# Kernel tuning notes

Hardware: AMD Instinct MI355X
Metric: run time of the kernel (lower is better)

The kernel has to match this reference:

```python
import jax, jax.numpy as jnp
import numpy as np

B, CIN, H, W = 4, 128, 160, 160
K = 100          # num instances
CH = 8           # mask head channels
OUT = 8          # mask branch out channels
STRIDE = 4
EPS = 1e-5


def conv3x3(x, w):
    # x: [B,C,H,W], w: [O,C,3,3] -> [B,O,H,W], stride 1, pad 1
    return jax.lax.conv_general_dilated(x, w, (1, 1), 'SAME',
                                        dimension_numbers=('NCHW', 'OIHW', 'NCHW'))


def setup_inputs() -> dict:
    key = jax.random.key(0)
    ks = jax.random.split(key, 6)
    cnn_feature = jax.random.normal(ks[0], (B, CIN, H, W), jnp.float32)
    tower_w = jax.random.normal(ks[1], (4, 128, 128, 3, 3), jnp.float32) * 0.03
    bn_gamma = jnp.ones((4, 128), jnp.float32)
    bn_beta = jnp.zeros((4, 128), jnp.float32)
    bn_mean = jnp.zeros((4, 128), jnp.float32)
    bn_var = jnp.ones((4, 128), jnp.float32)
    proj_w = jax.random.normal(ks[2], (OUT, 128), jnp.float32) * 0.05
    proj_b = jnp.zeros((OUT,), jnp.float32)
    ctrl_w = jax.random.normal(ks[3], (169, CIN, 3, 3), jnp.float32) * 0.01
    ctrl_b = jnp.zeros((169,), jnp.float32)
    detection = jax.random.randint(ks[4], (K, 2), 0, min(H, W), dtype=jnp.int32)
    return dict(cnn_feature=cnn_feature, tower_w=tower_w, bn_gamma=bn_gamma,
                bn_beta=bn_beta, bn_mean=bn_mean, bn_var=bn_var,
                proj_w=proj_w, proj_b=proj_b, ctrl_w=ctrl_w, ctrl_b=ctrl_b,
                detection=detection)


def reference(cnn_feature, tower_w, bn_gamma, bn_beta, bn_mean, bn_var,
              proj_w, proj_b, ctrl_w, ctrl_b, detection):
    x = cnn_feature
    for i in range(4):
        x = conv3x3(x, tower_w[i])
        inv = bn_gamma[i] / jnp.sqrt(bn_var[i] + EPS)            # [128]
        shift = bn_beta[i] - bn_mean[i] * inv
        x = jax.nn.relu(x * inv[None, :, None, None] + shift[None, :, None, None])
    mask_feats = jnp.einsum('bchw,oc->bohw', x, proj_w) + proj_b[None, :, None, None]

    # ----- controller: 3x3 conv producing 169 dynamic params per pixel -----
    ctrl = conv3x3(cnn_feature, ctrl_w) + ctrl_b[None, :, None, None]  # [B,169,H,W]

    # ----- gather per-instance params at detection centers (im_inds all 0) -----
    xs = detection[:, 0]
    ys = detection[:, 1]
    params = ctrl[0][:, ys, xs].T  # [K,169]

    # ----- relative coordinates -----
    sx = jnp.arange(W, dtype=jnp.float32) * STRIDE + STRIDE // 2
    sy = jnp.arange(H, dtype=jnp.float32) * STRIDE + STRIDE // 2
    gy, gx = jnp.meshgrid(sy, sx, indexing='ij')
    locations = jnp.stack([gx.reshape(-1), gy.reshape(-1)], axis=1)   # [HW,2]
    ct = detection.astype(jnp.float32) * STRIDE                        # [K,2]
    rel = (ct[:, None, :] - locations[None, :, :]).transpose(0, 2, 1)  # [K,2,HW]

    feats = jnp.broadcast_to(mask_feats[0].reshape(1, OUT, H * W), (K, OUT, H * W))
    h = jnp.concatenate([rel, feats], axis=1)  # [K,10,HW]

    # ----- parse dynamic params: weights first, then biases -----
    w0 = params[:, 0:80].reshape(K, CH, OUT + 2)     # (8+2)*8
    w1 = params[:, 80:144].reshape(K, CH, CH)        # 8*8
    w2 = params[:, 144:152].reshape(K, 1, CH)        # 8*1
    b0 = params[:, 152:160]
    b1 = params[:, 160:168]
    b2 = params[:, 168:169]

    # ----- dynamic grouped 1x1 convs == per-instance matmuls -----
    h = jax.nn.relu(jnp.einsum('koc,kcp->kop', w0, h) + b0[:, :, None])
    h = jax.nn.relu(jnp.einsum('koc,kcp->kop', w1, h) + b1[:, :, None])
    h = jnp.einsum('koc,kcp->kop', w2, h) + b2[:, :, None]  # [K,1,HW]
    return h.reshape(K, H, W)
```

## Files before the change

kernel.cpp:

```cpp
#include <hip/hip_runtime.h>
#include <hip/hip_bf16.h>

#define H 160
#define W 160
#define HW 25600
#define ROWB 40960

typedef __attribute__((ext_vector_type(8))) short bf16x8;
typedef __attribute__((ext_vector_type(4))) float f32x4;
typedef __attribute__((ext_vector_type(8))) unsigned short ushort8v;
typedef __attribute__((ext_vector_type(4))) unsigned short ushort4v;

typedef __attribute__((address_space(1))) const unsigned int gu32;
typedef __attribute__((address_space(3))) unsigned int lu32;

__device__ __forceinline__ void gload16(const void* g, void* l) {
    __builtin_amdgcn_global_load_lds((gu32*)g, (lu32*)l, 16, 0, 0);
}

__device__ __forceinline__ unsigned short f2b(float f) {
    unsigned int u = __float_as_uint(f);
    unsigned int r = (u + 0x7fffu + ((u >> 16) & 1u)) >> 16;
    return (unsigned short)r;
}
__device__ __forceinline__ float b2f(unsigned short b) {
    return __uint_as_float(((unsigned int)b) << 16);
}

#define LGKM0() asm volatile("s_waitcnt lgkmcnt(0)" ::: "memory")
#define BARRIER() asm volatile("s_barrier" ::: "memory")


__global__ __launch_bounds__(256) void fused_prep(
    const float* __restrict__ cnn,
    const float* __restrict__ tw,
    const float* __restrict__ gamma, const float* __restrict__ beta,
    const float* __restrict__ mean,  const float* __restrict__ var,
    const float* __restrict__ cw,
    char* __restrict__ actX, char* __restrict__ wbf,
    float* __restrict__ invshift, float* __restrict__ cwT)
{
    const int tid = threadIdx.x;
    const int b = blockIdx.x;

    if (b < 200) {
        int blk = b;
        int p0  = blk * 128 + (tid & 31) * 4;
        int cbh = tid >> 5;
#pragma unroll
        for (int pass = 0; pass < 2; ++pass) {
            int cb2 = pass * 8 + cbh;
            int ci0 = cb2 * 8;
            ushort8v o0, o1, o2, o3;
#pragma unroll
            for (int jj = 0; jj < 8; ++jj) {
                float4 v = *(const float4*)&cnn[(ci0 + jj) * HW + p0];
                o0[jj] = f2b(v.x);
                o1[jj] = f2b(v.y);
                o2[jj] = f2b(v.z);
                o3[jj] = f2b(v.w);
            }
            *(ushort8v*)(actX + (p0 + 0) * 256 + ((cb2 ^ ((p0 + 0) & 15)) * 16)) = o0;
            *(ushort8v*)(actX + (p0 + 1) * 256 + ((cb2 ^ ((p0 + 1) & 15)) * 16)) = o1;
            *(ushort8v*)(actX + (p0 + 2) * 256 + ((cb2 ^ ((p0 + 2) & 15)) * 16)) = o2;
            *(ushort8v*)(actX + (p0 + 3) * 256 + ((cb2 ^ ((p0 + 3) & 15)) * 16)) = o3;
        }
    } else if (b < 456) {
        int idx = (b - 200) * 256 + tid;
        int ci = idx & 127;
        int co = (idx >> 7) & 127;
        int l  = idx >> 14;
        int kk = ci >> 5;
        int cw2 = ci & 31;
        const float* src = tw + ((l * 128 + co) * 128 + ci) * 9;
        char* dst = wbf + l * 294912 + kk * 8192 + co * 64 + cw2 * 2;
#pragma unroll
        for (int t = 0; t < 9; ++t)
            *(unsigned short*)(dst + t * 32768) = f2b(src[t]);

        if (b == 200) {
            for (int c = tid; c < 512; c += 256) {
                int ll = c >> 7, ch = c & 127;
                float inv = gamma[ll * 128 + ch] * rsqrtf(var[ll * 128 + ch] + 1e-5f);
                float sh  = beta[ll * 128 + ch] - mean[ll * 128 + ch] * inv;
                invshift[ll * 256 + ch] = inv;
                invshift[ll * 256 + 128 + ch] = sh;
            }
        }
    } else {
        int idx = (b - 456) * 256 + tid;
        if (idx < 194688) {
            int j = idx / 169;
            int o = idx - j * 169;
            cwT[idx] = cw[o * 1152 + j];
        }
    }
}

template <int PROJ, int CTRL>
__global__ __launch_bounds__(512, 1) void conv_mfma(
    const char* __restrict__ actin,
    const char* __restrict__ wpl,
    const float* __restrict__ invshift_l,
    char* __restrict__ actout,
    const float* __restrict__ pw,
    const float* __restrict__ pb,
    float* __restrict__ mf,
    const float* __restrict__ cnn,
    const float* __restrict__ cwT,
    const float* __restrict__ cbp,
    const int*   __restrict__ det,
    float* __restrict__ params)
{
    __shared__ __align__(16) char smem[78848];

    const int tid  = threadIdx.x;

    if (CTRL && blockIdx.x >= 200) {
        float* patch = (float*)smem;
        float* sred  = (float*)(smem + 4608);
        const int k = blockIdx.x - 200;
        const int xk = det[2 * k];
        const int yk = det[2 * k + 1];
        for (int i = tid; i < 1152; i += 512) {
            int ci = i / 9;
            int rem = i - ci * 9;
            int r = rem / 3, s = rem - r * 3;
            int gy = yk + r - 1, gx = xk + s - 1;
            float v = 0.f;
            if ((unsigned)gy < (unsigned)H && (unsigned)gx < (unsigned)W)
                v = cnn[ci * HW + gy * W + gx];
            patch[i] = v;
        }
        __syncthreads();

        float acc = 0.f;
        if (tid < 507) {
            const int chunk = tid / 169;
            const int o = tid - chunk * 169;
            const int j0 = chunk * 384;
            const float* cp = cwT + o;
#pragma unroll 8
            for (int j = j0; j < j0 + 384; ++j)
                acc += cp[j * 169] * patch[j];
        }
        if (tid >= 169 && tid < 507) sred[tid - 169] = acc;
        __syncthreads();
        if (tid < 169)
            params[k * 169 + tid] = acc + sred[tid] + sred[169 + tid] + cbp[tid];
        return;
    }

    char* IT = smem;
    char* WQ = smem + 46080;

    const int lane = tid & 63;
    const int w    = tid >> 6;
    const int wp   = w >> 1;
    const int wc   = w & 1;
    const int g    = lane >> 4;
    const int i15  = lane & 15;

    const int bb = blockIdx.x;
    const int bx = bb % 10;
    const int by = bb / 10;
    const int tx0 = bx * 16 - 1;
    const int ty0 = by * 8 - 1;

    for (int it = 0; it < 6; ++it) {
        int c = it * 512 + tid;
        if (c < 2880) {
            int row  = c / 288;
            int rem  = c - row * 288;
            int px_i = rem >> 4;
            int bo   = (rem & 15) * 16;
            int cy = min(max(ty0 + row, 0), H - 1);
            int cx = min(max(tx0 + px_i, 0), W - 1);
            char* ldsb = IT + (it * 512 + (tid & ~63)) * 16;
            gload16(actin + cy * ROWB + cx * 256 + bo, ldsb);
        }
    }
#pragma unroll
    for (int pl = 0; pl < 3; ++pl)
        gload16(wpl + pl * 8192 + tid * 16,
                WQ + pl * 8192 + (tid & ~63) * 16);
    asm volatile("s_waitcnt vmcnt(2)" ::: "memory");
    for (int c = tid; c < 2880; c += 512) {
        int row  = c / 288;
        int rem  = c - row * 288;
        int px_i = rem >> 4;
        int gy = ty0 + row, gx = tx0 + px_i;
        if ((unsigned)gy >= (unsigned)H || (unsigned)gx >= (unsigned)W) {
            f32x4 z = {0.f, 0.f, 0.f, 0.f};
            *(f32x4*)(IT + c * 16) = z;
        }
    }
    LGKM0();
    BARRIER();

    f32x4 acc[4][2];
#pragma unroll
    for (int cf = 0; cf < 4; ++cf)
#pragma unroll
        for (int pf = 0; pf < 2; ++pf)
            acc[cf][pf] = (f32x4){0.f, 0.f, 0.f, 0.f};

#define CSTAGE(J, WN) {                                                        \
    if ((J) <= 32)                                                             \
        gload16(wpl + ((J) + 3) * 8192 + tid * 16,                             \
                WQ + (((J) + 3) & 3) * 8192 + (tid & ~63) * 16);               \
    asm volatile("s_waitcnt vmcnt(" #WN ")" ::: "memory");                     \
    {                                                                          \
        const int tap = (J) >> 2, kk = (J) & 3;                                \
        const int r = tap / 3, s = tap - r * 3;                                \
        const char* wbse = WQ + ((J) & 3) * 8192 + (wc * 64 + i15) * 64 + g * 16; \
        bf16x8 a0 = *(const bf16x8*)(wbse + 0 * 1024);                         \
        bf16x8 a1 = *(const bf16x8*)(wbse + 1 * 1024);                         \
        bf16x8 a2 = *(const bf16x8*)(wbse + 2 * 1024);                         \
        bf16x8 a3 = *(const bf16x8*)(wbse + 3 * 1024);                         \
        const int slotb = ((kk * 4 + g) ^ ((i15 + s + 15) & 15)) * 16;         \
        const char* ib = IT + (i15 + s) * 256 + slotb;                         \
        bf16x8 b0 = *(const bf16x8*)(ib + (wp * 2 + 0 + r) * 4608);            \
        bf16x8 b1 = *(const bf16x8*)(ib + (wp * 2 + 1 + r) * 4608);            \
        acc[0][0] = __builtin_amdgcn_mfma_f32_16x16x32_bf16(a0, b0, acc[0][0], 0, 0, 0); \
        acc[0][1] = __builtin_amdgcn_mfma_f32_16x16x32_bf16(a0, b1, acc[0][1], 0, 0, 0); \
        acc[1][0] = __builtin_amdgcn_mfma_f32_16x16x32_bf16(a1, b0, acc[1][0], 0, 0, 0); \
        acc[1][1] = __builtin_amdgcn_mfma_f32_16x16x32_bf16(a1, b1, acc[1][1], 0, 0, 0); \
        acc[2][0] = __builtin_amdgcn_mfma_f32_16x16x32_bf16(a2, b0, acc[2][0], 0, 0, 0); \
        acc[2][1] = __builtin_amdgcn_mfma_f32_16x16x32_bf16(a2, b1, acc[2][1], 0, 0, 0); \
        acc[3][0] = __builtin_amdgcn_mfma_f32_16x16x32_bf16(a3, b0, acc[3][0], 0, 0, 0); \
        acc[3][1] = __builtin_amdgcn_mfma_f32_16x16x32_bf16(a3, b1, acc[3][1], 0, 0, 0); \
    }                                                                          \
    BARRIER();                                                                 \
}

    CSTAGE(0,2)  CSTAGE(1,2)  CSTAGE(2,2)  CSTAGE(3,2)  CSTAGE(4,2)  CSTAGE(5,2)
    CSTAGE(6,2)  CSTAGE(7,2)  CSTAGE(8,2)  CSTAGE(9,2)  CSTAGE(10,2) CSTAGE(11,2)
    CSTAGE(12,2) CSTAGE(13,2) CSTAGE(14,2) CSTAGE(15,2) CSTAGE(16,2) CSTAGE(17,2)
    CSTAGE(18,2) CSTAGE(19,2) CSTAGE(20,2) CSTAGE(21,2) CSTAGE(22,2) CSTAGE(23,2)
    CSTAGE(24,2) CSTAGE(25,2) CSTAGE(26,2) CSTAGE(27,2) CSTAGE(28,2) CSTAGE(29,2)
    CSTAGE(30,2) CSTAGE(31,2) CSTAGE(32,2) CSTAGE(33,1) CSTAGE(34,0) CSTAGE(35,0)
#undef CSTAGE

    if (PROJ == 0) {
        const int gx = bx * 16 + i15;
#pragma unroll
        for (int cf = 0; cf < 4; ++cf) {
            int co0 = wc * 64 + cf * 16 + g * 4;
            int cbx = wc * 8 + cf * 2 + (g >> 1);
            int sbyte = ((cbx ^ i15) * 16) + (g & 1) * 8;
            f32x4 inv4 = *(const f32x4*)&invshift_l[co0];
            f32x4 sh4  = *(const f32x4*)&invshift_l[128 + co0];
#pragma unroll
            for (int pf = 0; pf < 2; ++pf) {
                int gy = by * 8 + wp * 2 + pf;
                f32x4 v = acc[cf][pf];
                ushort4v o;
                o.x = f2b(fmaxf(v.x * inv4.x + sh4.x, 0.f));
                o.y = f2b(fmaxf(v.y * inv4.y + sh4.y, 0.f));
                o.z = f2b(fmaxf(v.z * inv4.z + sh4.z, 0.f));
                o.w = f2b(fmaxf(v.w * inv4.w + sh4.w, 0.f));
                *(ushort4v*)(actout + gy * ROWB + gx * 256 + sbyte) = o;
            }
        }
    } else {
        char* actF = smem;
        float* spw = (float*)(smem + 32768);
        __syncthreads();
#pragma unroll
        for (int cf = 0; cf < 4; ++cf) {
            int co0 = wc * 64 + cf * 16 + g * 4;
            int cbx = wc * 8 + cf * 2 + (g >> 1);
            int sbyte = ((cbx ^ i15) * 16) + (g & 1) * 8;
            f32x4 inv4 = *(const f32x4*)&invshift_l[co0];
            f32x4 sh4  = *(const f32x4*)&invshift_l[128 + co0];
#pragma unroll
            for (int pf = 0; pf < 2; ++pf) {
                int px = (wp * 2 + pf) * 16 + i15;
                f32x4 v = acc[cf][pf];
                ushort4v o;
                o.x = f2b(fmaxf(v.x * inv4.x + sh4.x, 0.f));
                o.y = f2b(fmaxf(v.y * inv4.y + sh4.y, 0.f));
                o.z = f2b(fmaxf(v.z * inv4.z + sh4.z, 0.f));
                o.w = f2b(fmaxf(v.w * inv4.w + sh4.w, 0.f));
                *(ushort4v*)(actF + px * 256 + sbyte) = o;
            }
        }
        for (int i = tid; i < 1024; i += 512) spw[i] = pw[i];
        __syncthreads();
        int pxt = tid >> 2;
        int o0  = (tid & 3) * 2;
        float s0 = 0.f, s1 = 0.f;
#pragma unroll
        for (int cb2 = 0; cb2 < 16; ++cb2) {
            ushort8v vv = *(const ushort8v*)(actF + pxt * 256 + ((cb2 ^ (pxt & 15)) * 16));
#pragma unroll
            for (int j = 0; j < 8; ++j) {
                float f = b2f(vv[j]);
                int ci = cb2 * 8 + j;
                s0 += f * spw[o0 * 128 + ci];
                s1 += f * spw[(o0 + 1) * 128 + ci];
            }
        }
        int p = (by * 8 + (pxt >> 4)) * W + bx * 16 + (pxt & 15);
        mf[o0 * HW + p]       = s0 + pb[o0];
        mf[(o0 + 1) * HW + p] = s1 + pb[o0 + 1];
    }
}

__global__ __launch_bounds__(256) void head_kernel(
    const float* __restrict__ mf, const float* __restrict__ params,
    const int* __restrict__ det, float* __restrict__ out)
{
    __shared__ float sp[1690];
    __shared__ int sdet[20];
    const int tid = threadIdx.x;
    const int kg = blockIdx.y;
    for (int i = tid; i < 1690; i += 256) sp[i] = params[kg * 1690 + i];
    if (tid < 20) sdet[tid] = det[kg * 20 + tid];
    __syncthreads();

    const int p = blockIdx.x * 256 + tid;
    const int x = p % W;
    const int y = p / W;
    const float fx = (float)(x * 4 + 2);
    const float fy = (float)(y * 4 + 2);

    float f[8];
#pragma unroll
    for (int o = 0; o < 8; ++o) f[o] = mf[o * HW + p];

#pragma unroll 2
    for (int j = 0; j < 10; ++j) {
        const float* spj = &sp[j * 169];
        const float rel0 = (float)(sdet[2 * j] * 4) - fx;
        const float rel1 = (float)(sdet[2 * j + 1] * 4) - fy;
        float h0[8];
#pragma unroll
        for (int o = 0; o < 8; ++o) {
            float a = spj[152 + o] + spj[o * 10] * rel0 + spj[o * 10 + 1] * rel1;
#pragma unroll
            for (int c = 0; c < 8; ++c) a += spj[o * 10 + 2 + c] * f[c];
            h0[o] = fmaxf(a, 0.f);
        }
        float h1[8];
#pragma unroll
        for (int o = 0; o < 8; ++o) {
            float a = spj[160 + o];
#pragma unroll
            for (int c = 0; c < 8; ++c) a += spj[80 + o * 8 + c] * h0[c];
            h1[o] = fmaxf(a, 0.f);
        }
        float r = spj[168];
#pragma unroll
        for (int c = 0; c < 8; ++c) r += spj[144 + c] * h1[c];
        out[(kg * 10 + j) * HW + p] = r;
    }
}

extern "C" void kernel_launch(void* const* d_in, const int* in_sizes, int n_in,
                              void* d_out, int out_size, void* d_ws, size_t ws_size,
                              hipStream_t stream)
{
    const float* cnn    = (const float*)d_in[0];
    const float* towerw = (const float*)d_in[1];
    const float* gamma  = (const float*)d_in[2];
    const float* beta   = (const float*)d_in[3];
    const float* meanp  = (const float*)d_in[4];
    const float* varp   = (const float*)d_in[5];
    const float* projw  = (const float*)d_in[6];
    const float* projb  = (const float*)d_in[7];
    const float* ctrlw  = (const float*)d_in[8];
    const float* ctrlb  = (const float*)d_in[9];
    const int*   det    = (const int*)d_in[10];
    float* out = (float*)d_out;

    char*  outb     = (char*)d_out;
    char*  X        = outb;
    char*  wbf      = outb + 6553600;
    float* invshift = (float*)(outb + 7733248);
    float* cwT      = (float*)(outb + 7737344);

    char*  Y      = (char*)d_ws;
    float* mf     = (float*)((char*)d_ws + 6553600);
    float* params = (float*)((char*)d_ws + 7372800);

    fused_prep<<<dim3(1217), dim3(256), 0, stream>>>(
        cnn, towerw, gamma, beta, meanp, varp, ctrlw,
        X, wbf, invshift, cwT);

    conv_mfma<0, 1><<<dim3(300), dim3(512), 0, stream>>>(
        X, wbf + 0 * 294912, invshift + 0 * 256, Y,
        nullptr, nullptr, nullptr,
        cnn, cwT, ctrlb, det, params);
    conv_mfma<0, 0><<<dim3(200), dim3(512), 0, stream>>>(
        Y, wbf + 1 * 294912, invshift + 1 * 256, X,
        nullptr, nullptr, nullptr,
        nullptr, nullptr, nullptr, nullptr, nullptr);
    conv_mfma<0, 0><<<dim3(200), dim3(512), 0, stream>>>(
        X, wbf + 2 * 294912, invshift + 2 * 256, Y,
        nullptr, nullptr, nullptr,
        nullptr, nullptr, nullptr, nullptr, nullptr);
    conv_mfma<1, 0><<<dim3(200), dim3(512), 0, stream>>>(
        Y, wbf + 3 * 294912, invshift + 3 * 256, nullptr,
        projw, projb, mf,
        nullptr, nullptr, nullptr, nullptr, nullptr);

    head_kernel<<<dim3(100, 10), dim3(256), 0, stream>>>(mf, params, det, out);
}
```

Before: 103.9 us.

## Fuse dynamic mask head into last tower conv epilogue, drop head kernel

Folds the per-instance dynamic head computation into the epilogue of the final tower conv kernel. Mask features now stay in shared memory instead of round-tripping through global memory, and one kernel launch is removed. Because the output buffer is now written during that kernel, the layer-4 weights and BN params are moved into workspace so they are not overwritten. The trade-off is that the 200 conv blocks must each stream all 100 instance parameter sets, in five chunks separated by barriers, which serializes the head work onto fewer blocks.

```diff
diff --git a/kernel.cpp b/kernel.cpp
--- a/kernel.cpp
+++ b/kernel.cpp
@@ -38,7 +38,8 @@
     const float* __restrict__ mean,  const float* __restrict__ var,
     const float* __restrict__ cw,
     char* __restrict__ actX, char* __restrict__ wbf,
-    float* __restrict__ invshift, float* __restrict__ cwT)
+    float* __restrict__ invshift, float* __restrict__ cwT,
+    char* __restrict__ wbf4, float* __restrict__ invshift4)
 {
     const int tid = threadIdx.x;
     const int b = blockIdx.x;
@@ -73,7 +74,8 @@
         int kk = ci >> 5;
         int cw2 = ci & 31;
         const float* src = tw + ((l * 128 + co) * 128 + ci) * 9;
-        char* dst = wbf + l * 294912 + kk * 8192 + co * 64 + cw2 * 2;
+        char* base = (l < 3) ? (wbf + l * 294912) : wbf4;
+        char* dst = base + kk * 8192 + co * 64 + cw2 * 2;
 #pragma unroll
         for (int t = 0; t < 9; ++t)
             *(unsigned short*)(dst + t * 32768) = f2b(src[t]);
@@ -85,6 +87,10 @@
                 float sh  = beta[ll * 128 + ch] - mean[ll * 128 + ch] * inv;
                 invshift[ll * 256 + ch] = inv;
                 invshift[ll * 256 + 128 + ch] = sh;
+                if (ll == 3) {
+                    invshift4[ch] = inv;
+                    invshift4[128 + ch] = sh;
+                }
             }
         }
     } else {
@@ -105,12 +111,12 @@
     char* __restrict__ actout,
     const float* __restrict__ pw,
     const float* __restrict__ pb,
-    float* __restrict__ mf,
     const float* __restrict__ cnn,
     const float* __restrict__ cwT,
     const float* __restrict__ cbp,
     const int*   __restrict__ det,
-    float* __restrict__ params)
+    float* __restrict__ params,
+    float* __restrict__ outp)
 {
     __shared__ __align__(16) char smem[78848];
 
@@ -264,8 +270,11 @@
             }
         }
     } else {
-        char* actF = smem;
-        float* spw = (float*)(smem + 32768);
+        char* actF  = smem;
+        float* spw  = (float*)(smem + 32768);
+        float* pmf  = (float*)(smem + 36864);
+        float* spar = (float*)(smem + 40960);
+        int*   sdet = (int*)(smem + 54480);
         __syncthreads();
 #pragma unroll
         for (int cf = 0; cf < 4; ++cf) {
@@ -287,74 +296,71 @@
             }
         }
         for (int i = tid; i < 1024; i += 512) spw[i] = pw[i];
+        for (int i = tid; i < 200; i += 512) sdet[i] = det[i];
         __syncthreads();
-        int pxt = tid >> 2;
-        int o0  = (tid & 3) * 2;
-        float s0 = 0.f, s1 = 0.f;
-#pragma unroll
-        for (int cb2 = 0; cb2 < 16; ++cb2) {
-            ushort8v vv = *(const ushort8v*)(actF + pxt * 256 + ((cb2 ^ (pxt & 15)) * 16));
-#pragma unroll
-            for (int j = 0; j < 8; ++j) {
-                float f = b2f(vv[j]);
-                int ci = cb2 * 8 + j;
-                s0 += f * spw[o0 * 128 + ci];
-                s1 += f * spw[(o0 + 1) * 128 + ci];
-            }
-        }
-        int p = (by * 8 + (pxt >> 4)) * W + bx * 16 + (pxt & 15);
-        mf[o0 * HW + p]       = s0 + pb[o0];
-        mf[(o0 + 1) * HW + p] = s1 + pb[o0 + 1];
-    }
-}
-
-__global__ __launch_bounds__(256) void head_kernel(
-    const float* __restrict__ mf, const float* __restrict__ params,
-    const int* __restrict__ det, float* __restrict__ out)
-{
-    __shared__ float sp[1690];
-    __shared__ int sdet[20];
-    const int tid = threadIdx.x;
-    const int kg = blockIdx.y;
-    for (int i = tid; i < 1690; i += 256) sp[i] = params[kg * 1690 + i];
-    if (tid < 20) sdet[tid] = det[kg * 20 + tid];
-    __syncthreads();
-
-    const int p = blockIdx.x * 256 + tid;
-    const int x = p % W;
-    const int y = p / W;
-    const float fx = (float)(x * 4 + 2);
-    const float fy = (float)(y * 4 + 2);
-
-    float f[8];
-#pragma unroll
-    for (int o = 0; o < 8; ++o) f[o] = mf[o * HW + p];
-
-#pragma unroll 2
-    for (int j = 0; j < 10; ++j) {
-        const float* spj = &sp[j * 169];
-        const float rel0 = (float)(sdet[2 * j] * 4) - fx;
-        const float rel1 = (float)(sdet[2 * j + 1] * 4) - fy;
-        float h0[8];
-#pragma unroll
-        for (int o = 0; o < 8; ++o) {
-            float a = spj[152 + o] + spj[o * 10] * rel0 + spj[o * 10 + 1] * rel1;
-#pragma unroll
-            for (int c = 0; c < 8; ++c) a += spj[o * 10 + 2 + c] * f[c];
-            h0[o] = fmaxf(a, 0.f);
-        }
-        float h1[8];
-#pragma unroll
-        for (int o = 0; o < 8; ++o) {
-            float a = spj[160 + o];
-#pragma unroll
-            for (int c = 0; c < 8; ++c) a += spj[80 + o * 8 + c] * h0[c];
-            h1[o] = fmaxf(a, 0.f);
-        }
-        float r = spj[168];
-#pragma unroll
-        for (int c = 0; c < 8; ++c) r += spj[144 + c] * h1[c];
-        out[(kg * 10 + j) * HW + p] = r;
+        {
+            int pxt = tid >> 2;
+            int o0  = (tid & 3) * 2;
+            float s0 = 0.f, s1 = 0.f;
+#pragma unroll
+            for (int cb2 = 0; cb2 < 16; ++cb2) {
+                ushort8v vv = *(const ushort8v*)(actF + pxt * 256 + ((cb2 ^ (pxt & 15)) * 16));
+#pragma unroll
+                for (int j = 0; j < 8; ++j) {
+                    float fv = b2f(vv[j]);
+                    int ci = cb2 * 8 + j;
+                    s0 += fv * spw[o0 * 128 + ci];
+                    s1 += fv * spw[(o0 + 1) * 128 + ci];
+                }
+            }
+            pmf[pxt * 8 + o0]     = s0 + pb[o0];
+            pmf[pxt * 8 + o0 + 1] = s1 + pb[o0 + 1];
+        }
+        __syncthreads();
+        const int px  = tid >> 2;
+        const int kq  = tid & 3;
+        const int lx  = px & 15, ly = px >> 4;
+        const int gpx = (by * 8 + ly) * W + bx * 16 + lx;
+        const float fx = (float)((bx * 16 + lx) * 4 + 2);
+        const float fy = (float)((by * 8 + ly) * 4 + 2);
+        float f[8];
+#pragma unroll
+        for (int o = 0; o < 8; ++o) f[o] = pmf[px * 8 + o];
+
+        for (int chunk = 0; chunk < 5; ++chunk) {
+            for (int i = tid; i < 3380; i += 512)
+                spar[i] = params[chunk * 3380 + i];
+            __syncthreads();
+#pragma unroll
+            for (int jj = 0; jj < 5; ++jj) {
+                int kl = kq + jj * 4;
+                int k  = chunk * 20 + kl;
+                const float* spj = &spar[kl * 169];
+                float rel0 = (float)(sdet[2 * k] * 4) - fx;
+                float rel1 = (float)(sdet[2 * k + 1] * 4) - fy;
+                float h0[8];
+#pragma unroll
+                for (int o = 0; o < 8; ++o) {
+                    float a = spj[152 + o] + spj[o * 10] * rel0 + spj[o * 10 + 1] * rel1;
+#pragma unroll
+                    for (int c = 0; c < 8; ++c) a += spj[o * 10 + 2 + c] * f[c];
+                    h0[o] = fmaxf(a, 0.f);
+                }
+                float h1[8];
+#pragma unroll
+                for (int o = 0; o < 8; ++o) {
+                    float a = spj[160 + o];
+#pragma unroll
+                    for (int c = 0; c < 8; ++c) a += spj[80 + o * 8 + c] * h0[c];
+                    h1[o] = fmaxf(a, 0.f);
+                }
+                float r = spj[168];
+#pragma unroll
+                for (int c = 0; c < 8; ++c) r += spj[144 + c] * h1[c];
+                outp[k * HW + gpx] = r;
+            }
+            __syncthreads();
+        }
     }
 }
 
@@ -381,30 +387,29 @@
     float* invshift = (float*)(outb + 7733248);
     float* cwT      = (float*)(outb + 7737344);
 
-    char*  Y      = (char*)d_ws;
-    float* mf     = (float*)((char*)d_ws + 6553600);
-    float* params = (float*)((char*)d_ws + 7372800);
+    char*  Y         = (char*)d_ws;
+    char*  wbf4      = (char*)d_ws + 6553600;
+    float* invshift4 = (float*)((char*)d_ws + 6848512);
+    float* params    = (float*)((char*)d_ws + 7372800);
 
     fused_prep<<<dim3(1217), dim3(256), 0, stream>>>(
         cnn, towerw, gamma, beta, meanp, varp, ctrlw,
-        X, wbf, invshift, cwT);
+        X, wbf, invshift, cwT, wbf4, invshift4);
 
     conv_mfma<0, 1><<<dim3(300), dim3(512), 0, stream>>>(
         X, wbf + 0 * 294912, invshift + 0 * 256, Y,
-        nullptr, nullptr, nullptr,
-        cnn, cwT, ctrlb, det, params);
+        nullptr, nullptr,
+        cnn, cwT, ctrlb, det, params, nullptr);
     conv_mfma<0, 0><<<dim3(200), dim3(512), 0, stream>>>(
         Y, wbf + 1 * 294912, invshift + 1 * 256, X,
-        nullptr, nullptr, nullptr,
-        nullptr, nullptr, nullptr, nullptr, nullptr);
+        nullptr, nullptr,
+        nullptr, nullptr, nullptr, nullptr, nullptr, nullptr);
     conv_mfma<0, 0><<<dim3(200), dim3(512), 0, stream>>>(
         X, wbf + 2 * 294912, invshift + 2 * 256, Y,
-        nullptr, nullptr, nullptr,
-        nullptr, nullptr, nullptr, nullptr, nullptr);
+        nullptr, nullptr,
+        nullptr, nullptr, nullptr, nullptr, nullptr, nullptr);
     conv_mfma<1, 0><<<dim3(200), dim3(512), 0, stream>>>(
-        Y, wbf + 3 * 294912, invshift + 3 * 256, nullptr,
-        projw, projb, mf,
-        nullptr, nullptr, nullptr, nullptr, nullptr);
-
-    head_kernel<<<dim3(100, 10), dim3(256), 0, stream>>>(mf, params, det, out);
-}
+        Y, wbf4, invshift4, nullptr,
+        projw, projb,
+        nullptr, nullptr, nullptr, det, params, out);
+}
```

New measurement: 119.6 us. 1.15x slower.

## Double-buffer conv weight slices in pairs to halve barriers per K-loop

Applied to the files above, without the earlier changes.

Restructures the conv tower's weight pipeline. Each stage now consumes two 8KB weight slices, 18 stages instead of 36, and refills a two-slice half-buffer after the barrier instead of prefetching one slice before the wait. This halves the number of block-wide barriers and waitcnt points in the main MFMA loop. In exchange, prefetch lookahead becomes a coarser two-slice double buffer, which may expose more global-load latency per stage.

```diff
diff --git a/kernel.cpp b/kernel.cpp
--- a/kernel.cpp
+++ b/kernel.cpp
@@ -181,10 +181,10 @@
         }
     }
 #pragma unroll
-    for (int pl = 0; pl < 3; ++pl)
+    for (int pl = 0; pl < 4; ++pl)
         gload16(wpl + pl * 8192 + tid * 16,
                 WQ + pl * 8192 + (tid & ~63) * 16);
-    asm volatile("s_waitcnt vmcnt(2)" ::: "memory");
+    asm volatile("s_waitcnt vmcnt(4)" ::: "memory");
     for (int c = tid; c < 2880; c += 512) {
         int row  = c / 288;
         int rem  = c - row * 288;
@@ -205,42 +205,49 @@
         for (int pf = 0; pf < 2; ++pf)
             acc[cf][pf] = (f32x4){0.f, 0.f, 0.f, 0.f};
 
-#define CSTAGE(J, WN) {                                                        \
-    if ((J) <= 32)                                                             \
-        gload16(wpl + ((J) + 3) * 8192 + tid * 16,                             \
-                WQ + (((J) + 3) & 3) * 8192 + (tid & ~63) * 16);               \
+#define KKHALF(J, KKQ) {                                                       \
+    const int tap = (J) >> 1;                                                  \
+    const int r = tap / 3, s = tap - r * 3;                                    \
+    const int kk = (((J) & 1) << 1) + (KKQ);                                   \
+    const char* wbse = WQ + ((J) & 1) * 16384 + (KKQ) * 8192                   \
+                       + (wc * 64 + i15) * 64 + g * 16;                        \
+    bf16x8 a0 = *(const bf16x8*)(wbse + 0 * 1024);                             \
+    bf16x8 a1 = *(const bf16x8*)(wbse + 1 * 1024);                             \
+    bf16x8 a2 = *(const bf16x8*)(wbse + 2 * 1024);                             \
+    bf16x8 a3 = *(const bf16x8*)(wbse + 3 * 1024);                             \
+    const int slotb = ((kk * 4 + g) ^ ((i15 + s + 15) & 15)) * 16;             \
+    const char* ib = IT + (i15 + s) * 256 + slotb;                             \
+    bf16x8 b0 = *(const bf16x8*)(ib + (wp * 2 + 0 + r) * 4608);                \
+    bf16x8 b1 = *(const bf16x8*)(ib + (wp * 2 + 1 + r) * 4608);                \
+    acc[0][0] = __builtin_amdgcn_mfma_f32_16x16x32_bf16(a0, b0, acc[0][0], 0, 0, 0); \
+    acc[0][1] = __builtin_amdgcn_mfma_f32_16x16x32_bf16(a0, b1, acc[0][1], 0, 0, 0); \
+    acc[1][0] = __builtin_amdgcn_mfma_f32_16x16x32_bf16(a1, b0, acc[1][0], 0, 0, 0); \
+    acc[1][1] = __builtin_amdgcn_mfma_f32_16x16x32_bf16(a1, b1, acc[1][1], 0, 0, 0); \
+    acc[2][0] = __builtin_amdgcn_mfma_f32_16x16x32_bf16(a2, b0, acc[2][0], 0, 0, 0); \
+    acc[2][1] = __builtin_amdgcn_mfma_f32_16x16x32_bf16(a2, b1, acc[2][1], 0, 0, 0); \
+    acc[3][0] = __builtin_amdgcn_mfma_f32_16x16x32_bf16(a3, b0, acc[3][0], 0, 0, 0); \
+    acc[3][1] = __builtin_amdgcn_mfma_f32_16x16x32_bf16(a3, b1, acc[3][1], 0, 0, 0); \
+}
+
+#define CSTAGE2(J, WN) {                                                       \
     asm volatile("s_waitcnt vmcnt(" #WN ")" ::: "memory");                     \
-    {                                                                          \
-        const int tap = (J) >> 2, kk = (J) & 3;                                \
-        const int r = tap / 3, s = tap - r * 3;                                \
-        const char* wbse = WQ + ((J) & 3) * 8192 + (wc * 64 + i15) * 64 + g * 16; \
-        bf16x8 a0 = *(const bf16x8*)(wbse + 0 * 1024);                         \
-        bf16x8 a1 = *(const bf16x8*)(wbse + 1 * 1024);                         \
-        bf16x8 a2 = *(const bf16x8*)(wbse + 2 * 1024);                         \
-        bf16x8 a3 = *(const bf16x8*)(wbse + 3 * 1024);                         \
-        const int slotb = ((kk * 4 + g) ^ ((i15 + s + 15) & 15)) * 16;         \
-        const char* ib = IT + (i15 + s) * 256 + slotb;                         \
-        bf16x8 b0 = *(const bf16x8*)(ib + (wp * 2 + 0 + r) * 4608);            \
-        bf16x8 b1 = *(const bf16x8*)(ib + (wp * 2 + 1 + r) * 4608);            \
-        acc[0][0] = __builtin_amdgcn_mfma_f32_16x16x32_bf16(a0, b0, acc[0][0], 0, 0, 0); \
-        acc[0][1] = __builtin_amdgcn_mfma_f32_16x16x32_bf16(a0, b1, acc[0][1], 0, 0, 0); \
-        acc[1][0] = __builtin_amdgcn_mfma_f32_16x16x32_bf16(a1, b0, acc[1][0], 0, 0, 0); \
-        acc[1][1] = __builtin_amdgcn_mfma_f32_16x16x32_bf16(a1, b1, acc[1][1], 0, 0, 0); \
-        acc[2][0] = __builtin_amdgcn_mfma_f32_16x16x32_bf16(a2, b0, acc[2][0], 0, 0, 0); \
-        acc[2][1] = __builtin_amdgcn_mfma_f32_16x16x32_bf16(a2, b1, acc[2][1], 0, 0, 0); \
-        acc[3][0] = __builtin_amdgcn_mfma_f32_16x16x32_bf16(a3, b0, acc[3][0], 0, 0, 0); \
-        acc[3][1] = __builtin_amdgcn_mfma_f32_16x16x32_bf16(a3, b1, acc[3][1], 0, 0, 0); \
+    KKHALF(J, 0)                                                               \
+    KKHALF(J, 1)                                                               \
+    BARRIER();                                                                 \
+    if ((J) <= 15) {                                                           \
+        const char* src = wpl + ((J) * 2 + 4) * 8192;                          \
+        char* dst = WQ + ((J) & 1) * 16384;                                    \
+        gload16(src + tid * 16,        dst + (tid & ~63) * 16);                \
+        gload16(src + 8192 + tid * 16, dst + 8192 + (tid & ~63) * 16);         \
     }                                                                          \
-    BARRIER();                                                                 \
-}
-
-    CSTAGE(0,2)  CSTAGE(1,2)  CSTAGE(2,2)  CSTAGE(3,2)  CSTAGE(4,2)  CSTAGE(5,2)
-    CSTAGE(6,2)  CSTAGE(7,2)  CSTAGE(8,2)  CSTAGE(9,2)  CSTAGE(10,2) CSTAGE(11,2)
-    CSTAGE(12,2) CSTAGE(13,2) CSTAGE(14,2) CSTAGE(15,2) CSTAGE(16,2) CSTAGE(17,2)
-    CSTAGE(18,2) CSTAGE(19,2) CSTAGE(20,2) CSTAGE(21,2) CSTAGE(22,2) CSTAGE(23,2)
-    CSTAGE(24,2) CSTAGE(25,2) CSTAGE(26,2) CSTAGE(27,2) CSTAGE(28,2) CSTAGE(29,2)
-    CSTAGE(30,2) CSTAGE(31,2) CSTAGE(32,2) CSTAGE(33,1) CSTAGE(34,0) CSTAGE(35,0)
-#undef CSTAGE
+}
+
+    CSTAGE2(0,2)  CSTAGE2(1,2)  CSTAGE2(2,2)  CSTAGE2(3,2)  CSTAGE2(4,2)
+    CSTAGE2(5,2)  CSTAGE2(6,2)  CSTAGE2(7,2)  CSTAGE2(8,2)  CSTAGE2(9,2)
+    CSTAGE2(10,2) CSTAGE2(11,2) CSTAGE2(12,2) CSTAGE2(13,2) CSTAGE2(14,2)
+    CSTAGE2(15,2) CSTAGE2(16,2) CSTAGE2(17,0)
+#undef CSTAGE2
+#undef KKHALF
 
     if (PROJ == 0) {
         const int gx = bx * 16 + i15;
```

Result: no change. 102.3 us (-1.6%).
